# Kernel tuning notes

Measured on AMD Instinct MI355X. Metric: run time of the kernel, lower is better.

The kernel has to match this reference:

```python
import jax, jax.numpy as jnp
import numpy as np

N_NODES = 50000
N_EDGES = 400000
MUL0 = 16   # multiplicity of 0e irreps (scalars)
MUL1 = 8    # multiplicity of 1o irreps (vectors)
IN_DIM = MUL0 + 3 * MUL1          # 40
EDGE_FEAT = 32
W00 = MUL0 * MUL0                 # 0e x 0e -> 0e : 256
W10 = MUL1 * MUL1                 # 1o x 0e -> 1o : 64
W01 = MUL0 * MUL1                 # 0e x 1o -> 1o : 128
W11 = MUL1 * MUL0                 # 1o x 1o -> 0e : 128
WEIGHT_NUMEL = W00 + W10 + W01 + W11  # 576
INV_SQRT3 = 1.0 / np.sqrt(3.0).astype(np.float32)
# e3nn 'component' normalization with path_normalization='element':
# fan_in into each output irrep = sum over paths of mul1*mul2 = 16+8 = 24
ALPHA0 = np.float32(np.sqrt(1.0 / 24.0))  # sqrt((2*0+1)/fan_in)
ALPHA1 = np.float32(np.sqrt(3.0 / 24.0))  # sqrt((2*1+1)/fan_in)


def setup_inputs() -> dict:
    key = jax.random.key(0)
    ks = jax.random.split(key, 10)
    node_attr = jax.random.normal(ks[0], (N_NODES, IN_DIM), dtype=jnp.float32)
    edge_index = jax.random.randint(ks[1], (2, N_EDGES), 0, N_NODES, dtype=jnp.int32)
    edge_attr = jax.random.normal(ks[2], (N_EDGES, EDGE_FEAT), dtype=jnp.float32)
    edge_sh = jax.random.normal(ks[3], (N_EDGES, 4), dtype=jnp.float32)
    s = 1.0 / np.sqrt(EDGE_FEAT)
    w1 = jax.random.normal(ks[4], (EDGE_FEAT, EDGE_FEAT), dtype=jnp.float32) * s
    b1 = jnp.zeros((EDGE_FEAT,), dtype=jnp.float32)
    w2 = jax.random.normal(ks[5], (EDGE_FEAT, WEIGHT_NUMEL), dtype=jnp.float32) * s
    b2 = jnp.zeros((WEIGHT_NUMEL,), dtype=jnp.float32)
    return {"node_attr": node_attr, "edge_index": edge_index, "edge_attr": edge_attr,
            "edge_sh": edge_sh, "w1": w1, "b1": b1, "w2": w2, "b2": b2}


def _tp_conv(node_attr, edge_index, edge_attr, edge_sh, w1, b1, w2, b2):
    edge_src, edge_dst = edge_index[0], edge_index[1]
    # edge MLP -> per-edge tensor-product weights [E, 576]
    h = jax.nn.softplus(edge_attr @ w1 + b1)
    w = h @ w2 + b2
    w00 = w[:, :W00].reshape(-1, MUL0, MUL0)
    w10 = w[:, W00:W00 + W10].reshape(-1, MUL1, MUL1)
    w01 = w[:, W00 + W10:W00 + W10 + W01].reshape(-1, MUL0, MUL1)
    w11 = w[:, W00 + W10 + W01:].reshape(-1, MUL1, MUL0)
    # gather source features (node_attr[edge_dst]) and split irreps
    x = node_attr[edge_dst]                       # [E, 40]
    s0 = x[:, :MUL0]                              # [E, 16]  scalars 0e
    v1 = x[:, MUL0:].reshape(-1, MUL1, 3)         # [E, 8, 3] vectors 1o
    y0 = edge_sh[:, 0]                            # [E]      sh l=0
    y1 = edge_sh[:, 1:4]                          # [E, 3]   sh l=1
    # CG tensor product paths (unit-norm wigner 3j):
    # 0e x 0e -> 0e (w3j = 1) and 1o x 1o -> 0e (w3j = eps-free delta/sqrt3)
    out0 = ALPHA0 * (jnp.einsum('eu,e,euw->ew', s0, y0, w00)
                     + INV_SQRT3 * jnp.einsum('eum,em,euw->ew', v1, y1, w11))
    # 1o x 0e -> 1o and 0e x 1o -> 1o (w3j = delta/sqrt3)
    out1 = ALPHA1 * INV_SQRT3 * (jnp.einsum('eum,e,euw->ewm', v1, y0, w10)
                                 + jnp.einsum('eu,em,euw->ewm', s0, y1, w01))
    tp = jnp.concatenate([out0, out1.reshape(-1, 3 * MUL1)], axis=-1)  # [E, 40]
    # scatter-mean over edge_src
    n = node_attr.shape[0]
    summed = jax.ops.segment_sum(tp, edge_src, num_segments=n)
    counts = jax.ops.segment_sum(jnp.ones((tp.shape[0],), tp.dtype), edge_src, num_segments=n)
    out = summed / jnp.maximum(counts, 1.0)[:, None]
    # residual (out_dim == in_dim, so F.pad is a no-op)
    return out + node_attr


def reference(node_attr, edge_index, edge_attr, edge_sh, w1, b1, w2, b2):
    return _tp_conv(node_attr, edge_index, edge_attr, edge_sh, w1, b1, w2, b2)
```

## Files before the change

kernel.cpp:

```cpp
#include <hip/hip_runtime.h>
#include <hip/hip_bf16.h>
#include <math.h>

#define NNODES 50000
#define NEDGES 400000
#define ALPHA0f    0.20412414523193154f
#define INV_SQRT3f 0.57735026918962576f
#define TPROW      64

typedef short bf16x8 __attribute__((ext_vector_type(8)));
typedef float f32x4  __attribute__((ext_vector_type(4)));
typedef float f32x16 __attribute__((ext_vector_type(16)));
typedef unsigned int u32x4 __attribute__((ext_vector_type(4)));

__device__ __forceinline__ short f2bf(float x) {
    __hip_bfloat16 h = __float2bfloat16(x);
    return *reinterpret_cast<short*>(&h);
}
__device__ __forceinline__ unsigned f2bfu(float x) {
    __hip_bfloat16 h = __float2bfloat16(x);
    return (unsigned)*reinterpret_cast<unsigned short*>(&h);
}
__device__ __forceinline__ float bf2f(unsigned short x) {
    return __uint_as_float(((unsigned)x) << 16);
}
__device__ __forceinline__ unsigned pack2(float a, float b) {
    return f2bfu(a) | (f2bfu(b) << 16);
}
__device__ __forceinline__ float softplus_f(float x) {
    return fmaxf(x, 0.0f) + __logf(1.0f + __expf(-fabsf(x)));
}

template<int MODE>
__global__ __launch_bounds__(512)
void tp_mfma_kernel(const float* __restrict__ node_attr,
                    const int*   __restrict__ edge_index,
                    const float* __restrict__ edge_attr,
                    const float* __restrict__ edge_sh,
                    const float* __restrict__ w1,
                    const float* __restrict__ b1,
                    const float* __restrict__ w2,
                    const float* __restrict__ b2,
                    unsigned short* __restrict__ tp_out,
                    int*   __restrict__ counts_i,
                    float* __restrict__ summed,
                    float* __restrict__ counts)
{
    __shared__ short w2f[18 * 2 * 512];
    __shared__ float b1s[32];
    __shared__ float b2s[576];
    __shared__ unsigned short xsb[8][32][44];

    const int tid = threadIdx.x;

    for (int i = tid; i < 18432; i += 512) {
        int col = i % 576, k = i / 576;
        int t = col >> 5, lr = col & 31, kh = k >> 4, lg = (k >> 3) & 1, j = k & 7;
        w2f[(((t * 2 + kh) * 64) + (lr | (lg << 5))) * 8 + j] = f2bf(w2[i]);
    }
    if (tid < 32) b1s[tid] = b1[tid];
    for (int i = tid; i < 576; i += 512) b2s[i] = b2[i];
    __syncthreads();

    const int wid = tid >> 6, lane = tid & 63;
    const int le = lane & 31, s = lane >> 5;

    bf16x8 w1a0, w1a1;
    #pragma unroll
    for (int j = 0; j < 8; ++j) {
        w1a0[j] = f2bf(w1[(s * 8 + j) * 32 + le]);
        w1a1[j] = f2bf(w1[(16 + s * 8 + j) * 32 + le]);
    }
    bf16x8 ab;
    #pragma unroll
    for (int j = 0; j < 8; ++j) {
        int u = s * 8 + j;
        float v = (le < 16) ? b2[u * 16 + le]
                : (le < 24) ? b2[320 + u * 8 + (le - 16)] : 0.0f;
        ab[j] = f2bf(v);
    }
    f32x16 zero16;
    #pragma unroll
    for (int i = 0; i < 16; ++i) zero16[i] = 0.0f;

    const int NGROUPS = (NEDGES + 255) / 256;

    for (int g = blockIdx.x; g < NGROUPS; g += gridDim.x) {
        const int e0 = g * 256 + wid * 32;
        if (e0 >= NEDGES) continue;

        int dval = (lane < 32) ? edge_index[NEDGES + e0 + lane] : 0;
        #pragma unroll
        for (int it = 0; it < 5; ++it) {
            int c = it * 64 + lane;
            int row = c / 10, part = c % 10;
            int d = __shfl(dval, row);
            float4 v = *(const float4*)(node_attr + (size_t)d * 40 + part * 4);
            short4 sx;
            sx.x = f2bf(v.x); sx.y = f2bf(v.y); sx.z = f2bf(v.z); sx.w = f2bf(v.w);
            *(short4*)&xsb[wid][row][part * 4] = sx;
        }
        const float4 sh = *(const float4*)(edge_sh + (size_t)(e0 + le) * 4);
        const float y0 = sh.x, y1x = sh.y, y1y = sh.z, y1z = sh.w;
        const int srcv = edge_index[e0 + le];

        const float* ear = edge_attr + (size_t)(e0 + le) * 32;
        bf16x8 bf1a, bf1b;
        {
            float4 a0 = *(const float4*)(ear + s * 8);
            float4 a1 = *(const float4*)(ear + s * 8 + 4);
            float4 b0 = *(const float4*)(ear + 16 + s * 8);
            float4 b1v = *(const float4*)(ear + 16 + s * 8 + 4);
            bf1a[0]=f2bf(a0.x); bf1a[1]=f2bf(a0.y); bf1a[2]=f2bf(a0.z); bf1a[3]=f2bf(a0.w);
            bf1a[4]=f2bf(a1.x); bf1a[5]=f2bf(a1.y); bf1a[6]=f2bf(a1.z); bf1a[7]=f2bf(a1.w);
            bf1b[0]=f2bf(b0.x); bf1b[1]=f2bf(b0.y); bf1b[2]=f2bf(b0.z); bf1b[3]=f2bf(b0.w);
            bf1b[4]=f2bf(b1v.x); bf1b[5]=f2bf(b1v.y); bf1b[6]=f2bf(b1v.z); bf1b[7]=f2bf(b1v.w);
        }
        f32x16 c1 = __builtin_amdgcn_mfma_f32_32x32x16_bf16(w1a0, bf1a, zero16, 0, 0, 0);
        c1 = __builtin_amdgcn_mfma_f32_32x32x16_bf16(w1a1, bf1b, c1, 0, 0, 0);

        unsigned P[8];
        #pragma unroll
        for (int q = 0; q < 8; ++q) {
            int r0 = 2 * q, r1 = 2 * q + 1;
            int j0 = (r0 & 3) + 8 * (r0 >> 2) + 4 * s;
            int j1 = (r1 & 3) + 8 * (r1 >> 2) + 4 * s;
            P[q] = pack2(softplus_f(c1[r0] + b1s[j0]), softplus_f(c1[r1] + b1s[j1]));
        }
        unsigned x0 = (unsigned)__shfl_xor((int)(s ? P[0] : P[2]), 32);
        unsigned x1 = (unsigned)__shfl_xor((int)(s ? P[1] : P[3]), 32);
        unsigned x2 = (unsigned)__shfl_xor((int)(s ? P[4] : P[6]), 32);
        unsigned x3 = (unsigned)__shfl_xor((int)(s ? P[5] : P[7]), 32);
        u32x4 hw0, hw1;
        hw0[0] = s ? x0 : P[0];  hw0[1] = s ? x1 : P[1];
        hw0[2] = s ? P[2] : x0;  hw0[3] = s ? P[3] : x1;
        hw1[0] = s ? x2 : P[4];  hw1[1] = s ? x3 : P[5];
        hw1[2] = s ? P[6] : x2;  hw1[3] = s ? P[7] : x3;
        const bf16x8 hf0 = *reinterpret_cast<bf16x8*>(&hw0);
        const bf16x8 hf1 = *reinterpret_cast<bf16x8*>(&hw1);

        bf16x8 s0f;
        {
            short4 a = *(const short4*)&xsb[wid][le][s * 8];
            short4 b = *(const short4*)&xsb[wid][le][s * 8 + 4];
            s0f[0]=a.x; s0f[1]=a.y; s0f[2]=a.z; s0f[3]=a.w;
            s0f[4]=b.x; s0f[5]=b.y; s0f[6]=b.z; s0f[7]=b.w;
        }
        f32x16 dbias = __builtin_amdgcn_mfma_f32_32x32x16_bf16(ab, s0f, zero16, 0, 0, 0);

        float acc0[8], r01[4], am0[4], am1[4], am2[4];
        #pragma unroll
        for (int i = 0; i < 8; ++i) acc0[i] = dbias[i] * y0;
        #pragma unroll
        for (int i = 0; i < 4; ++i) { r01[i] = dbias[8 + i];
                                      am0[i] = 0.f; am1[i] = 0.f; am2[i] = 0.f; }

        #pragma unroll 2
        for (int t = 0; t < 8; ++t) {
            bf16x8 wa0 = *reinterpret_cast<const bf16x8*>(&w2f[((t * 2 + 0) * 64 + lane) * 8]);
            bf16x8 wa1 = *reinterpret_cast<const bf16x8*>(&w2f[((t * 2 + 1) * 64 + lane) * 8]);
            f32x16 wv = __builtin_amdgcn_mfma_f32_32x32x16_bf16(wa0, hf0, zero16, 0, 0, 0);
            wv = __builtin_amdgcn_mfma_f32_32x32x16_bf16(wa1, hf1, wv, 0, 0, 0);
            float F0 = bf2f(xsb[wid][le][2 * t])     * y0;
            float F1 = bf2f(xsb[wid][le][2 * t + 1]) * y0;
            #pragma unroll
            for (int r = 0; r < 8; ++r) acc0[r] += wv[r] * F0;
            #pragma unroll
            for (int r = 0; r < 8; ++r) acc0[r] += wv[8 + r] * F1;
        }
        #pragma unroll 1
        for (int tt = 0; tt < 2; ++tt) {
            int tb = (8 + tt) * 2;
            bf16x8 wa0 = *reinterpret_cast<const bf16x8*>(&w2f[((tb + 0) * 64 + lane) * 8]);
            bf16x8 wa1 = *reinterpret_cast<const bf16x8*>(&w2f[((tb + 1) * 64 + lane) * 8]);
            f32x16 wv = __builtin_amdgcn_mfma_f32_32x32x16_bf16(wa0, hf0, zero16, 0, 0, 0);
            wv = __builtin_amdgcn_mfma_f32_32x32x16_bf16(wa1, hf1, wv, 0, 0, 0);
            #pragma unroll
            for (int q = 0; q < 4; ++q) {
                int u = 4 * tt + q;
                float f0 = y0 * bf2f(xsb[wid][le][16 + u * 3 + 0]);
                float f1 = y0 * bf2f(xsb[wid][le][16 + u * 3 + 1]);
                float f2 = y0 * bf2f(xsb[wid][le][16 + u * 3 + 2]);
                f32x4 b2q = *(const f32x4*)&b2s[256 + tt * 32 + 8 * q + 4 * s];
                #pragma unroll
                for (int k = 0; k < 4; ++k) {
                    float wb = wv[4 * q + k] + b2q[k];
                    am0[k] += wb * f0; am1[k] += wb * f1; am2[k] += wb * f2;
                }
            }
        }
        #pragma unroll 1
        for (int tt = 0; tt < 4; ++tt) {
            int tb = (10 + tt) * 2;
            bf16x8 wa0 = *reinterpret_cast<const bf16x8*>(&w2f[((tb + 0) * 64 + lane) * 8]);
            bf16x8 wa1 = *reinterpret_cast<const bf16x8*>(&w2f[((tb + 1) * 64 + lane) * 8]);
            f32x16 wv = __builtin_amdgcn_mfma_f32_32x32x16_bf16(wa0, hf0, zero16, 0, 0, 0);
            wv = __builtin_amdgcn_mfma_f32_32x32x16_bf16(wa1, hf1, wv, 0, 0, 0);
            #pragma unroll
            for (int q = 0; q < 4; ++q) {
                float su = bf2f(xsb[wid][le][4 * tt + q]);
                #pragma unroll
                for (int k = 0; k < 4; ++k) r01[k] += wv[4 * q + k] * su;
            }
        }
        #pragma unroll 1
        for (int tt = 0; tt < 4; ++tt) {
            int tb = (14 + tt) * 2;
            bf16x8 wa0 = *reinterpret_cast<const bf16x8*>(&w2f[((tb + 0) * 64 + lane) * 8]);
            bf16x8 wa1 = *reinterpret_cast<const bf16x8*>(&w2f[((tb + 1) * 64 + lane) * 8]);
            f32x16 wv = __builtin_amdgcn_mfma_f32_32x32x16_bf16(wa0, hf0, zero16, 0, 0, 0);
            wv = __builtin_amdgcn_mfma_f32_32x32x16_bf16(wa1, hf1, wv, 0, 0, 0);
            int u0 = 2 * tt, u1 = 2 * tt + 1;
            float bu0 = INV_SQRT3f * (bf2f(xsb[wid][le][16 + u0 * 3 + 0]) * y1x +
                                      bf2f(xsb[wid][le][16 + u0 * 3 + 1]) * y1y +
                                      bf2f(xsb[wid][le][16 + u0 * 3 + 2]) * y1z);
            float bu1 = INV_SQRT3f * (bf2f(xsb[wid][le][16 + u1 * 3 + 0]) * y1x +
                                      bf2f(xsb[wid][le][16 + u1 * 3 + 1]) * y1y +
                                      bf2f(xsb[wid][le][16 + u1 * 3 + 2]) * y1z);
            f32x4 bq0 = *(const f32x4*)&b2s[448 + tt * 32 + 4 * s];
            f32x4 bq1 = *(const f32x4*)&b2s[448 + tt * 32 + 8 + 4 * s];
            f32x4 bq2 = *(const f32x4*)&b2s[448 + tt * 32 + 16 + 4 * s];
            f32x4 bq3 = *(const f32x4*)&b2s[448 + tt * 32 + 24 + 4 * s];
            #pragma unroll
            for (int k = 0; k < 4; ++k) {
                acc0[k]     += (wv[k]      + bq0[k]) * bu0;
                acc0[4 + k] += (wv[4 + k]  + bq1[k]) * bu0;
                acc0[k]     += (wv[8 + k]  + bq2[k]) * bu1;
                acc0[4 + k] += (wv[12 + k] + bq3[k]) * bu1;
            }
        }

        float o1[12];
        #pragma unroll
        for (int w = 0; w < 4; ++w) {
            o1[w * 3 + 0] = ALPHA0f * (am0[w] + y1x * r01[w]);
            o1[w * 3 + 1] = ALPHA0f * (am1[w] + y1y * r01[w]);
            o1[w * 3 + 2] = ALPHA0f * (am2[w] + y1z * r01[w]);
        }
        if (MODE == 1) {
            unsigned short* rowp = tp_out + (size_t)(e0 + le) * TPROW;
            short4 sa, sb;
            sa.x = f2bf(ALPHA0f * acc0[0]); sa.y = f2bf(ALPHA0f * acc0[1]);
            sa.z = f2bf(ALPHA0f * acc0[2]); sa.w = f2bf(ALPHA0f * acc0[3]);
            sb.x = f2bf(ALPHA0f * acc0[4]); sb.y = f2bf(ALPHA0f * acc0[5]);
            sb.z = f2bf(ALPHA0f * acc0[6]); sb.w = f2bf(ALPHA0f * acc0[7]);
            *(short4*)(rowp + 4 * s)     = sa;
            *(short4*)(rowp + 8 + 4 * s) = sb;
            #pragma unroll
            for (int q = 0; q < 3; ++q) {
                short4 sq;
                sq.x = f2bf(o1[q * 4 + 0]); sq.y = f2bf(o1[q * 4 + 1]);
                sq.z = f2bf(o1[q * 4 + 2]); sq.w = f2bf(o1[q * 4 + 3]);
                *(short4*)(rowp + 16 + 12 * s + q * 4) = sq;
            }
            if (s == 0) atomicAdd(&counts_i[srcv], 1);
        } else {
            float* row = summed + (size_t)srcv * 40;
            #pragma unroll
            for (int i = 0; i < 4; ++i) {
                atomicAdd(row + i + 4 * s,     ALPHA0f * acc0[i]);
                atomicAdd(row + 8 + i + 4 * s, ALPHA0f * acc0[4 + i]);
            }
            #pragma unroll
            for (int q = 0; q < 12; ++q)
                atomicAdd(row + 16 + 12 * s + q, o1[q]);
            if (s == 0) atomicAdd(&counts[srcv], 1.0f);
        }
    }
}

extern "C" __global__ __launch_bounds__(256)
void scanA_kernel(const int* __restrict__ counts_i, int* __restrict__ offsets,
                  int* __restrict__ bsums)
{
    __shared__ int sm[256];
    int t = threadIdx.x, id = blockIdx.x * 256 + t;
    int c = (id < NNODES) ? counts_i[id] : 0;
    sm[t] = c; __syncthreads();
    #pragma unroll
    for (int off = 1; off < 256; off <<= 1) {
        int v = (t >= off) ? sm[t - off] : 0;
        __syncthreads();
        sm[t] += v;
        __syncthreads();
    }
    if (id < NNODES) offsets[id] = sm[t] - c;
    if (t == 255) bsums[blockIdx.x] = sm[255];
}

extern "C" __global__ __launch_bounds__(256)
void scanB_kernel(int* __restrict__ bsums, int nblocks)
{
    __shared__ int sm[256];
    int t = threadIdx.x;
    int c = (t < nblocks) ? bsums[t] : 0;
    sm[t] = c; __syncthreads();
    #pragma unroll
    for (int off = 1; off < 256; off <<= 1) {
        int v = (t >= off) ? sm[t - off] : 0;
        __syncthreads();
        sm[t] += v;
        __syncthreads();
    }
    if (t < nblocks) bsums[t] = sm[t] - c;
}

extern "C" __global__ __launch_bounds__(256)
void scanC_kernel(int* __restrict__ offsets, const int* __restrict__ bsums,
                  int* __restrict__ cursor)
{
    int id = blockIdx.x * 256 + threadIdx.x;
    if (id < NNODES) {
        int o = offsets[id] + bsums[id >> 8];
        offsets[id] = o;
        cursor[id] = o;
    }
}

extern "C" __global__ __launch_bounds__(256)
void scatter_kernel(const int* __restrict__ edge_index, int* __restrict__ cursor,
                    int* __restrict__ csr)
{
    int e = blockIdx.x * 256 + threadIdx.x;
    if (e < NEDGES) {
        int src = edge_index[e];
        int pos = atomicAdd(&cursor[src], 1);
        csr[pos] = e;
    }
}

extern "C" __global__ __launch_bounds__(256)
void gather_kernel(const unsigned short* __restrict__ tp, const int* __restrict__ offsets,
                   const int* __restrict__ csr, const float* __restrict__ node_attr,
                   float* __restrict__ out)
{
    int gw = (blockIdx.x * 256 + threadIdx.x) >> 6;
    int lane = threadIdx.x & 63;
    int nwaves = (gridDim.x * 256) >> 6;
    for (int n = gw; n < NNODES; n += nwaves) {
        int start = offsets[n];
        int end = (n + 1 < NNODES) ? offsets[n + 1] : NEDGES;
        float a0 = 0.f, a1 = 0.f, a2 = 0.f, a3 = 0.f;
        int i = start;
        for (; i + 8 <= end; i += 8) {
            int i0 = csr[i],     i1 = csr[i + 1], i2 = csr[i + 2], i3 = csr[i + 3];
            int i4 = csr[i + 4], i5 = csr[i + 5], i6 = csr[i + 6], i7 = csr[i + 7];
            if (lane < 40) {
                a0 += bf2f(tp[(size_t)i0 * TPROW + lane]);
                a1 += bf2f(tp[(size_t)i1 * TPROW + lane]);
                a2 += bf2f(tp[(size_t)i2 * TPROW + lane]);
                a3 += bf2f(tp[(size_t)i3 * TPROW + lane]);
                a0 += bf2f(tp[(size_t)i4 * TPROW + lane]);
                a1 += bf2f(tp[(size_t)i5 * TPROW + lane]);
                a2 += bf2f(tp[(size_t)i6 * TPROW + lane]);
                a3 += bf2f(tp[(size_t)i7 * TPROW + lane]);
            }
        }
        for (; i + 2 <= end; i += 2) {
            int i0 = csr[i], i1 = csr[i + 1];
            if (lane < 40) {
                a0 += bf2f(tp[(size_t)i0 * TPROW + lane]);
                a1 += bf2f(tp[(size_t)i1 * TPROW + lane]);
            }
        }
        if (i < end) {
            int i0 = csr[i];
            if (lane < 40) a0 += bf2f(tp[(size_t)i0 * TPROW + lane]);
        }
        if (lane < 40) {
            float deg = (float)(end - start);
            out[(size_t)n * 40 + lane] =
                ((a0 + a1) + (a2 + a3)) / fmaxf(deg, 1.0f) + node_attr[(size_t)n * 40 + lane];
        }
    }
}

extern "C" __global__ __launch_bounds__(256)
void finalize_kernel(const float* __restrict__ summed,
                     const float* __restrict__ counts,
                     const float* __restrict__ node_attr,
                     float* __restrict__ out)
{
    int idx = blockIdx.x * 256 + threadIdx.x;
    if (idx < NNODES * 40) {
        int n = idx / 40;
        float c = fmaxf(counts[n], 1.0f);
        out[idx] = summed[idx] / c + node_attr[idx];
    }
}

extern "C" void kernel_launch(void* const* d_in, const int* in_sizes, int n_in,
                              void* d_out, int out_size, void* d_ws, size_t ws_size,
                              hipStream_t stream)
{
    const float* node_attr  = (const float*)d_in[0];
    const int*   edge_index = (const int*)  d_in[1];
    const float* edge_attr  = (const float*)d_in[2];
    const float* edge_sh    = (const float*)d_in[3];
    const float* w1 = (const float*)d_in[4];
    const float* b1 = (const float*)d_in[5];
    const float* w2 = (const float*)d_in[6];
    const float* b2 = (const float*)d_in[7];
    float* out = (float*)d_out;

    const int SCAN_BLOCKS = (NNODES + 255) / 256;
    const int EDGE_BLOCKS = (NEDGES + 255) / 256;
    const size_t NEED = (size_t)NEDGES * TPROW * 2 +
                        ((size_t)3 * NNODES + NEDGES + 256) * 4;

    if (ws_size >= NEED) {
        unsigned short* tp = (unsigned short*)d_ws;
        int* counts_i = (int*)(tp + (size_t)NEDGES * TPROW);
        int* offsets  = counts_i + NNODES;
        int* cursor   = offsets + NNODES;
        int* csr      = cursor + NNODES;
        int* bsums    = csr + NEDGES;

        hipMemsetAsync(counts_i, 0, (size_t)NNODES * 4, stream);

        hipLaunchKernelGGL((tp_mfma_kernel<1>), dim3(512), dim3(512), 0, stream,
                           node_attr, edge_index, edge_attr, edge_sh, w1, b1, w2, b2,
                           tp, counts_i, (float*)nullptr, (float*)nullptr);

        hipLaunchKernelGGL(scanA_kernel, dim3(SCAN_BLOCKS), dim3(256), 0, stream,
                           counts_i, offsets, bsums);
        hipLaunchKernelGGL(scanB_kernel, dim3(1), dim3(256), 0, stream,
                           bsums, SCAN_BLOCKS);
        hipLaunchKernelGGL(scanC_kernel, dim3(SCAN_BLOCKS), dim3(256), 0, stream,
                           offsets, bsums, cursor);
        hipLaunchKernelGGL(scatter_kernel, dim3(EDGE_BLOCKS), dim3(256), 0, stream,
                           edge_index, cursor, csr);
        hipLaunchKernelGGL(gather_kernel, dim3(2048), dim3(256), 0, stream,
                           tp, offsets, csr, node_attr, out);
    } else {
        float* summed = (float*)d_ws;
        float* counts = summed + (size_t)NNODES * 40;
        hipMemsetAsync(d_ws, 0, (size_t)(NNODES * 40 + NNODES) * sizeof(float), stream);
        hipLaunchKernelGGL((tp_mfma_kernel<0>), dim3(512), dim3(512), 0, stream,
                           node_attr, edge_index, edge_attr, edge_sh, w1, b1, w2, b2,
                           (unsigned short*)nullptr, (int*)nullptr, summed, counts);
        int fblk = (NNODES * 40 + 255) / 256;
        hipLaunchKernelGGL(finalize_kernel, dim3(fblk), dim3(256), 0, stream,
                           summed, counts, node_attr, out);
    }
}
```

Baseline: 117.8 us.

## Fuse CSR build into one cooperative kernel and move counting out of TP kernel

Replaces the memset, three scan kernels and scatter kernel with a single cooperative kernel that zeroes counts, histograms edge sources, scans and scatters, separated by grid-wide syncs. The per-edge count atomics are removed from the tensor-product kernel, which now runs after CSR construction. This cuts launch count and per-kernel gaps, in exchange for grid.sync costs and running a 196-block grid with strided loops over edges.

```diff
diff --git a/kernel.cpp b/kernel.cpp
--- a/kernel.cpp
+++ b/kernel.cpp
@@ -1,12 +1,16 @@
 #include <hip/hip_runtime.h>
 #include <hip/hip_bf16.h>
+#include <hip/hip_cooperative_groups.h>
 #include <math.h>
+
+namespace cg = cooperative_groups;
 
 #define NNODES 50000
 #define NEDGES 400000
 #define ALPHA0f    0.20412414523193154f
 #define INV_SQRT3f 0.57735026918962576f
 #define TPROW      64
+#define SCAN_BLOCKS 196
 
 typedef short bf16x8 __attribute__((ext_vector_type(8)));
 typedef float f32x4  __attribute__((ext_vector_type(4)));
@@ -42,7 +46,6 @@
                     const float* __restrict__ w2,
                     const float* __restrict__ b2,
                     unsigned short* __restrict__ tp_out,
-                    int*   __restrict__ counts_i,
                     float* __restrict__ summed,
                     float* __restrict__ counts)
 {
@@ -102,7 +105,6 @@
         }
         const float4 sh = *(const float4*)(edge_sh + (size_t)(e0 + le) * 4);
         const float y0 = sh.x, y1x = sh.y, y1y = sh.z, y1z = sh.w;
-        const int srcv = edge_index[e0 + le];
 
         const float* ear = edge_attr + (size_t)(e0 + le) * 32;
         bf16x8 bf1a, bf1b;
@@ -253,8 +255,8 @@
                 sq.z = f2bf(o1[q * 4 + 2]); sq.w = f2bf(o1[q * 4 + 3]);
                 *(short4*)(rowp + 16 + 12 * s + q * 4) = sq;
             }
-            if (s == 0) atomicAdd(&counts_i[srcv], 1);
         } else {
+            const int srcv = edge_index[e0 + le];
             float* row = summed + (size_t)srcv * 40;
             #pragma unroll
             for (int i = 0; i < 4; ++i) {
@@ -270,59 +272,55 @@
 }
 
 extern "C" __global__ __launch_bounds__(256)
-void scanA_kernel(const int* __restrict__ counts_i, int* __restrict__ offsets,
-                  int* __restrict__ bsums)
+void csr_build_kernel(const int* __restrict__ edge_index,
+                      int* __restrict__ counts_i, int* __restrict__ offsets,
+                      int* __restrict__ cursor, int* __restrict__ csr,
+                      int* __restrict__ bsums)
 {
+    cg::grid_group grid = cg::this_grid();
     __shared__ int sm[256];
-    int t = threadIdx.x, id = blockIdx.x * 256 + t;
-    int c = (id < NNODES) ? counts_i[id] : 0;
-    sm[t] = c; __syncthreads();
-    #pragma unroll
-    for (int off = 1; off < 256; off <<= 1) {
-        int v = (t >= off) ? sm[t - off] : 0;
-        __syncthreads();
-        sm[t] += v;
-        __syncthreads();
-    }
-    if (id < NNODES) offsets[id] = sm[t] - c;
-    if (t == 255) bsums[blockIdx.x] = sm[255];
-}
-
-extern "C" __global__ __launch_bounds__(256)
-void scanB_kernel(int* __restrict__ bsums, int nblocks)
-{
-    __shared__ int sm[256];
-    int t = threadIdx.x;
-    int c = (t < nblocks) ? bsums[t] : 0;
-    sm[t] = c; __syncthreads();
-    #pragma unroll
-    for (int off = 1; off < 256; off <<= 1) {
-        int v = (t >= off) ? sm[t - off] : 0;
-        __syncthreads();
-        sm[t] += v;
-        __syncthreads();
-    }
-    if (t < nblocks) bsums[t] = sm[t] - c;
-}
-
-extern "C" __global__ __launch_bounds__(256)
-void scanC_kernel(int* __restrict__ offsets, const int* __restrict__ bsums,
-                  int* __restrict__ cursor)
-{
-    int id = blockIdx.x * 256 + threadIdx.x;
-    if (id < NNODES) {
-        int o = offsets[id] + bsums[id >> 8];
-        offsets[id] = o;
-        cursor[id] = o;
-    }
-}
-
-extern "C" __global__ __launch_bounds__(256)
-void scatter_kernel(const int* __restrict__ edge_index, int* __restrict__ cursor,
-                    int* __restrict__ csr)
-{
-    int e = blockIdx.x * 256 + threadIdx.x;
-    if (e < NEDGES) {
+    const int t = threadIdx.x;
+    const int gid = blockIdx.x * 256 + t;
+    const int gsz = gridDim.x * 256;
+
+    for (int i = gid; i < NNODES; i += gsz) counts_i[i] = 0;
+    grid.sync();
+    for (int e = gid; e < NEDGES; e += gsz) atomicAdd(&counts_i[edge_index[e]], 1);
+    grid.sync();
+    {
+        int c = (gid < NNODES) ? counts_i[gid] : 0;
+        sm[t] = c; __syncthreads();
+        #pragma unroll
+        for (int off = 1; off < 256; off <<= 1) {
+            int v = (t >= off) ? sm[t - off] : 0;
+            __syncthreads();
+            sm[t] += v;
+            __syncthreads();
+        }
+        if (gid < NNODES) offsets[gid] = sm[t] - c;
+        if (t == 255) bsums[blockIdx.x] = sm[255];
+    }
+    grid.sync();
+    if (blockIdx.x == 0) {
+        int c = (t < gridDim.x) ? bsums[t] : 0;
+        sm[t] = c; __syncthreads();
+        #pragma unroll
+        for (int off = 1; off < 256; off <<= 1) {
+            int v = (t >= off) ? sm[t - off] : 0;
+            __syncthreads();
+            sm[t] += v;
+            __syncthreads();
+        }
+        if (t < gridDim.x) bsums[t] = sm[t] - c;
+    }
+    grid.sync();
+    if (gid < NNODES) {
+        int o = offsets[gid] + bsums[blockIdx.x];
+        offsets[gid] = o;
+        cursor[gid] = o;
+    }
+    grid.sync();
+    for (int e = gid; e < NEDGES; e += gsz) {
         int src = edge_index[e];
         int pos = atomicAdd(&cursor[src], 1);
         csr[pos] = e;
@@ -403,8 +401,6 @@
     const float* b2 = (const float*)d_in[7];
     float* out = (float*)d_out;
 
-    const int SCAN_BLOCKS = (NNODES + 255) / 256;
-    const int EDGE_BLOCKS = (NEDGES + 255) / 256;
     const size_t NEED = (size_t)NEDGES * TPROW * 2 +
                         ((size_t)3 * NNODES + NEDGES + 256) * 4;
 
@@ -416,20 +412,15 @@
         int* csr      = cursor + NNODES;
         int* bsums    = csr + NEDGES;
 
-        hipMemsetAsync(counts_i, 0, (size_t)NNODES * 4, stream);
+        void* args[] = {(void*)&edge_index, (void*)&counts_i, (void*)&offsets,
+                        (void*)&cursor, (void*)&csr, (void*)&bsums};
+        hipLaunchCooperativeKernel((const void*)csr_build_kernel,
+                                   dim3(SCAN_BLOCKS), dim3(256), args, 0, stream);
 
         hipLaunchKernelGGL((tp_mfma_kernel<1>), dim3(512), dim3(512), 0, stream,
                            node_attr, edge_index, edge_attr, edge_sh, w1, b1, w2, b2,
-                           tp, counts_i, (float*)nullptr, (float*)nullptr);
-
-        hipLaunchKernelGGL(scanA_kernel, dim3(SCAN_BLOCKS), dim3(256), 0, stream,
-                           counts_i, offsets, bsums);
-        hipLaunchKernelGGL(scanB_kernel, dim3(1), dim3(256), 0, stream,
-                           bsums, SCAN_BLOCKS);
-        hipLaunchKernelGGL(scanC_kernel, dim3(SCAN_BLOCKS), dim3(256), 0, stream,
-                           offsets, bsums, cursor);
-        hipLaunchKernelGGL(scatter_kernel, dim3(EDGE_BLOCKS), dim3(256), 0, stream,
-                           edge_index, cursor, csr);
+                           tp, (float*)nullptr, (float*)nullptr);
+
         hipLaunchKernelGGL(gather_kernel, dim3(2048), dim3(256), 0, stream,
                            tp, offsets, csr, node_attr, out);
     } else {
@@ -438,7 +429,7 @@
         hipMemsetAsync(d_ws, 0, (size_t)(NNODES * 40 + NNODES) * sizeof(float), stream);
         hipLaunchKernelGGL((tp_mfma_kernel<0>), dim3(512), dim3(512), 0, stream,
                            node_attr, edge_index, edge_attr, edge_sh, w1, b1, w2, b2,
-                           (unsigned short*)nullptr, (int*)nullptr, summed, counts);
+                           (unsigned short*)nullptr, summed, counts);
         int fblk = (NNODES * 40 + 255) / 256;
         hipLaunchKernelGGL(finalize_kernel, dim3(fblk), dim3(256), 0, stream,
                            summed, counts, node_attr, out);
```

Result: slower. 239.4 us (+103.2%).

## Keep gathered node features in registers instead of LDS and fully unroll loops

Applied to the files above, without the earlier changes.

Each lane now loads its edge's full 40-float node row directly and packs it to bf16 in 20 registers, replacing the cooperative LDS staging buffer xsb and its per-iteration LDS reads. All inner weight loops are fully unrolled, and the grid doubles to 1024 blocks. The aim is to remove LDS traffic and free shared memory so more blocks fit per CU. In exchange, VGPR pressure rises and the global loads become uncoalesced per-lane row reads. The src index load moves to the point of use.

```diff
diff --git a/kernel.cpp b/kernel.cpp
--- a/kernel.cpp
+++ b/kernel.cpp
@@ -30,6 +30,8 @@
 __device__ __forceinline__ float softplus_f(float x) {
     return fmaxf(x, 0.0f) + __logf(1.0f + __expf(-fabsf(x)));
 }
+#define XV(xp, j) (((j) & 1) ? __uint_as_float((xp)[(j) >> 1] & 0xffff0000u) \
+                             : __uint_as_float((xp)[(j) >> 1] << 16))
 
 template<int MODE>
 __global__ __launch_bounds__(512)
@@ -49,7 +51,6 @@
     __shared__ short w2f[18 * 2 * 512];
     __shared__ float b1s[32];
     __shared__ float b2s[576];
-    __shared__ unsigned short xsb[8][32][44];
 
     const int tid = threadIdx.x;
 
@@ -89,20 +90,19 @@
         const int e0 = g * 256 + wid * 32;
         if (e0 >= NEDGES) continue;
 
-        int dval = (lane < 32) ? edge_index[NEDGES + e0 + lane] : 0;
-        #pragma unroll
-        for (int it = 0; it < 5; ++it) {
-            int c = it * 64 + lane;
-            int row = c / 10, part = c % 10;
-            int d = __shfl(dval, row);
-            float4 v = *(const float4*)(node_attr + (size_t)d * 40 + part * 4);
-            short4 sx;
-            sx.x = f2bf(v.x); sx.y = f2bf(v.y); sx.z = f2bf(v.z); sx.w = f2bf(v.w);
-            *(short4*)&xsb[wid][row][part * 4] = sx;
+        const int dval = edge_index[NEDGES + e0 + le];
+        unsigned xp[20];
+        {
+            const float* xr = node_attr + (size_t)dval * 40;
+            #pragma unroll
+            for (int i = 0; i < 10; ++i) {
+                float4 v = *(const float4*)(xr + i * 4);
+                xp[i * 2]     = pack2(v.x, v.y);
+                xp[i * 2 + 1] = pack2(v.z, v.w);
+            }
         }
         const float4 sh = *(const float4*)(edge_sh + (size_t)(e0 + le) * 4);
         const float y0 = sh.x, y1x = sh.y, y1y = sh.z, y1z = sh.w;
-        const int srcv = edge_index[e0 + le];
 
         const float* ear = edge_attr + (size_t)(e0 + le) * 32;
         bf16x8 bf1a, bf1b;
@@ -141,10 +141,10 @@
 
         bf16x8 s0f;
         {
-            short4 a = *(const short4*)&xsb[wid][le][s * 8];
-            short4 b = *(const short4*)&xsb[wid][le][s * 8 + 4];
-            s0f[0]=a.x; s0f[1]=a.y; s0f[2]=a.z; s0f[3]=a.w;
-            s0f[4]=b.x; s0f[5]=b.y; s0f[6]=b.z; s0f[7]=b.w;
+            u32x4 sw;
+            sw[0] = xp[4 * s]; sw[1] = xp[4 * s + 1];
+            sw[2] = xp[4 * s + 2]; sw[3] = xp[4 * s + 3];
+            s0f = *reinterpret_cast<bf16x8*>(&sw);
         }
         f32x16 dbias = __builtin_amdgcn_mfma_f32_32x32x16_bf16(ab, s0f, zero16, 0, 0, 0);
 
@@ -155,20 +155,20 @@
         for (int i = 0; i < 4; ++i) { r01[i] = dbias[8 + i];
                                       am0[i] = 0.f; am1[i] = 0.f; am2[i] = 0.f; }
 
-        #pragma unroll 2
+        #pragma unroll
         for (int t = 0; t < 8; ++t) {
             bf16x8 wa0 = *reinterpret_cast<const bf16x8*>(&w2f[((t * 2 + 0) * 64 + lane) * 8]);
             bf16x8 wa1 = *reinterpret_cast<const bf16x8*>(&w2f[((t * 2 + 1) * 64 + lane) * 8]);
             f32x16 wv = __builtin_amdgcn_mfma_f32_32x32x16_bf16(wa0, hf0, zero16, 0, 0, 0);
             wv = __builtin_amdgcn_mfma_f32_32x32x16_bf16(wa1, hf1, wv, 0, 0, 0);
-            float F0 = bf2f(xsb[wid][le][2 * t])     * y0;
-            float F1 = bf2f(xsb[wid][le][2 * t + 1]) * y0;
+            float F0 = XV(xp, 2 * t) * y0;
+            float F1 = XV(xp, 2 * t + 1) * y0;
             #pragma unroll
             for (int r = 0; r < 8; ++r) acc0[r] += wv[r] * F0;
             #pragma unroll
             for (int r = 0; r < 8; ++r) acc0[r] += wv[8 + r] * F1;
         }
-        #pragma unroll 1
+        #pragma unroll
         for (int tt = 0; tt < 2; ++tt) {
             int tb = (8 + tt) * 2;
             bf16x8 wa0 = *reinterpret_cast<const bf16x8*>(&w2f[((tb + 0) * 64 + lane) * 8]);
@@ -178,9 +178,9 @@
             #pragma unroll
             for (int q = 0; q < 4; ++q) {
                 int u = 4 * tt + q;
-                float f0 = y0 * bf2f(xsb[wid][le][16 + u * 3 + 0]);
-                float f1 = y0 * bf2f(xsb[wid][le][16 + u * 3 + 1]);
-                float f2 = y0 * bf2f(xsb[wid][le][16 + u * 3 + 2]);
+                float f0 = y0 * XV(xp, 16 + u * 3 + 0);
+                float f1 = y0 * XV(xp, 16 + u * 3 + 1);
+                float f2 = y0 * XV(xp, 16 + u * 3 + 2);
                 f32x4 b2q = *(const f32x4*)&b2s[256 + tt * 32 + 8 * q + 4 * s];
                 #pragma unroll
                 for (int k = 0; k < 4; ++k) {
@@ -189,7 +189,7 @@
                 }
             }
         }
-        #pragma unroll 1
+        #pragma unroll
         for (int tt = 0; tt < 4; ++tt) {
             int tb = (10 + tt) * 2;
             bf16x8 wa0 = *reinterpret_cast<const bf16x8*>(&w2f[((tb + 0) * 64 + lane) * 8]);
@@ -198,12 +198,12 @@
             wv = __builtin_amdgcn_mfma_f32_32x32x16_bf16(wa1, hf1, wv, 0, 0, 0);
             #pragma unroll
             for (int q = 0; q < 4; ++q) {
-                float su = bf2f(xsb[wid][le][4 * tt + q]);
+                float su = XV(xp, 4 * tt + q);
                 #pragma unroll
                 for (int k = 0; k < 4; ++k) r01[k] += wv[4 * q + k] * su;
             }
         }
-        #pragma unroll 1
+        #pragma unroll
         for (int tt = 0; tt < 4; ++tt) {
             int tb = (14 + tt) * 2;
             bf16x8 wa0 = *reinterpret_cast<const bf16x8*>(&w2f[((tb + 0) * 64 + lane) * 8]);
@@ -211,12 +211,12 @@
             f32x16 wv = __builtin_amdgcn_mfma_f32_32x32x16_bf16(wa0, hf0, zero16, 0, 0, 0);
             wv = __builtin_amdgcn_mfma_f32_32x32x16_bf16(wa1, hf1, wv, 0, 0, 0);
             int u0 = 2 * tt, u1 = 2 * tt + 1;
-            float bu0 = INV_SQRT3f * (bf2f(xsb[wid][le][16 + u0 * 3 + 0]) * y1x +
-                                      bf2f(xsb[wid][le][16 + u0 * 3 + 1]) * y1y +
-                                      bf2f(xsb[wid][le][16 + u0 * 3 + 2]) * y1z);
-            float bu1 = INV_SQRT3f * (bf2f(xsb[wid][le][16 + u1 * 3 + 0]) * y1x +
-                                      bf2f(xsb[wid][le][16 + u1 * 3 + 1]) * y1y +
-                                      bf2f(xsb[wid][le][16 + u1 * 3 + 2]) * y1z);
+            float bu0 = INV_SQRT3f * (XV(xp, 16 + u0 * 3 + 0) * y1x +
+                                      XV(xp, 16 + u0 * 3 + 1) * y1y +
+                                      XV(xp, 16 + u0 * 3 + 2) * y1z);
+            float bu1 = INV_SQRT3f * (XV(xp, 16 + u1 * 3 + 0) * y1x +
+                                      XV(xp, 16 + u1 * 3 + 1) * y1y +
+                                      XV(xp, 16 + u1 * 3 + 2) * y1z);
             f32x4 bq0 = *(const f32x4*)&b2s[448 + tt * 32 + 4 * s];
             f32x4 bq1 = *(const f32x4*)&b2s[448 + tt * 32 + 8 + 4 * s];
             f32x4 bq2 = *(const f32x4*)&b2s[448 + tt * 32 + 16 + 4 * s];
@@ -253,8 +253,9 @@
                 sq.z = f2bf(o1[q * 4 + 2]); sq.w = f2bf(o1[q * 4 + 3]);
                 *(short4*)(rowp + 16 + 12 * s + q * 4) = sq;
             }
-            if (s == 0) atomicAdd(&counts_i[srcv], 1);
+            if (s == 0) atomicAdd(&counts_i[edge_index[e0 + le]], 1);
         } else {
+            const int srcv = edge_index[e0 + le];
             float* row = summed + (size_t)srcv * 40;
             #pragma unroll
             for (int i = 0; i < 4; ++i) {
@@ -418,7 +419,7 @@
 
         hipMemsetAsync(counts_i, 0, (size_t)NNODES * 4, stream);
 
-        hipLaunchKernelGGL((tp_mfma_kernel<1>), dim3(512), dim3(512), 0, stream,
+        hipLaunchKernelGGL((tp_mfma_kernel<1>), dim3(1024), dim3(512), 0, stream,
                            node_attr, edge_index, edge_attr, edge_sh, w1, b1, w2, b2,
                            tp, counts_i, (float*)nullptr, (float*)nullptr);
 
@@ -436,7 +437,7 @@
         float* summed = (float*)d_ws;
         float* counts = summed + (size_t)NNODES * 40;
         hipMemsetAsync(d_ws, 0, (size_t)(NNODES * 40 + NNODES) * sizeof(float), stream);
-        hipLaunchKernelGGL((tp_mfma_kernel<0>), dim3(512), dim3(512), 0, stream,
+        hipLaunchKernelGGL((tp_mfma_kernel<0>), dim3(1024), dim3(512), 0, stream,
                            node_attr, edge_index, edge_attr, edge_sh, w1, b1, w2, b2,
                            (unsigned short*)nullptr, (int*)nullptr, summed, counts);
         int fblk = (NNODES * 40 + 255) / 256;
```

New measurement: 132.5 us. 12.4% more time.
